# Kernel tuning notes

Hardware: AMD Instinct MI355X
Metric: run time of the kernel (lower is better)

Reference implementation:

```python
import jax, jax.numpy as jnp
import numpy as np

N = 50000      # nodes
E = 800000     # edges
F_IN = 128     # input_channels
H = 128        # hidden_channels
OUT = 10       # output_channels
G = 64         # graphs in batch


def setup_inputs() -> dict:
    key = jax.random.key(0)
    ks = jax.random.split(key, 16)
    s = 0.05
    inp = {
        "x": jax.random.normal(ks[0], (N, F_IN), jnp.float32),
        "edge_index": jax.random.randint(ks[1], (2, E), 0, N, jnp.int64 if jax.config.jax_enable_x64 else jnp.int32),
        "batch": jnp.sort(jax.random.randint(ks[2], (N,), 0, G, jnp.int32)),
        "conv1_w": jax.random.normal(ks[3], (F_IN, H), jnp.float32) * s,
        "conv1_b": jnp.zeros((H,), jnp.float32),
        "conv2_w": jax.random.normal(ks[4], (H, H), jnp.float32) * s,
        "conv2_b": jnp.zeros((H,), jnp.float32),
        "conv3_w": jax.random.normal(ks[5], (H, H), jnp.float32) * s,
        "conv3_b": jnp.zeros((H,), jnp.float32),
        "fc1_w": jax.random.normal(ks[6], (H, 8 * H), jnp.float32) * s,
        "fc1_b": jnp.zeros((8 * H,), jnp.float32),
        "fc2_w": jax.random.normal(ks[7], (8 * H, 4 * H), jnp.float32) * s,
        "fc2_b": jnp.zeros((4 * H,), jnp.float32),
        "fc3_w": jax.random.normal(ks[8], (4 * H, 2 * H), jnp.float32) * s,
        "fc3_b": jnp.zeros((2 * H,), jnp.float32),
        "fc4_w": jax.random.normal(ks[9], (2 * H, H), jnp.float32) * s,
        "fc4_b": jnp.zeros((H,), jnp.float32),
        "fc5_w": jax.random.normal(ks[10], (H, OUT), jnp.float32) * s,
        "fc5_b": jnp.zeros((OUT,), jnp.float32),
    }
    return inp


def _gcn_conv(x, w, b, src, dst, norm, n_nodes):
    # GCNConv: out = D^{-1/2} (A + I) D^{-1/2} X W + b   (self-loops already in src/dst)
    xw = x @ w                                        # [N, H]
    msg = xw[src] * norm[:, None]                     # gather + scale, [E+N, H]
    return jax.ops.segment_sum(msg, dst, num_segments=n_nodes) + b


def reference(x, edge_index, batch,
              conv1_w, conv1_b, conv2_w, conv2_b, conv3_w, conv3_b,
              fc1_w, fc1_b, fc2_w, fc2_b, fc3_w, fc3_b,
              fc4_w, fc4_b, fc5_w, fc5_b):
    n = x.shape[0]
    loop = jnp.arange(n, dtype=edge_index.dtype)
    src = jnp.concatenate([edge_index[0], loop])      # add self-loops
    dst = jnp.concatenate([edge_index[1], loop])
    deg = jax.ops.segment_sum(jnp.ones_like(dst, dtype=x.dtype), dst, num_segments=n)
    dinv = jnp.where(deg > 0, jax.lax.rsqrt(deg), 0.0)
    norm = dinv[src] * dinv[dst]                      # symmetric normalization per edge

    h = jax.nn.relu(_gcn_conv(x, conv1_w, conv1_b, src, dst, norm, n))
    h = jax.nn.relu(_gcn_conv(h, conv2_w, conv2_b, src, dst, norm, n))
    h = _gcn_conv(h, conv3_w, conv3_b, src, dst, norm, n)

    # global mean pool over graphs
    sums = jax.ops.segment_sum(h, batch, num_segments=G)
    cnt = jax.ops.segment_sum(jnp.ones((n,), x.dtype), batch, num_segments=G)
    f = sums / jnp.maximum(cnt, 1.0)[:, None]         # [G, H]

    y = jax.nn.relu(f @ fc1_w + fc1_b)
    y = jax.nn.relu(y @ fc2_w + fc2_b)
    y = jax.nn.relu(y @ fc3_w + fc3_b)
    y = jax.nn.relu(y @ fc4_w + fc4_b)
    # dropout p=0.5 is identity in eval mode
    y = y @ fc5_w + fc5_b                             # [G, OUT]
    return (f, y)
```

## Files before the change

### kernel.cpp

```cpp
#include <hip/hip_runtime.h>
#include <stdint.h>

#define N_NODES 50000
#define N_EDGES 800000
#define FEAT    128
#define NGRAPH  64

#define E_BLKS      3125
#define GSTRIP_BLKS 782
#define GR_BLKS     (GSTRIP_BLKS + E_BLKS)

typedef __attribute__((ext_vector_type(8))) short short8;
typedef __attribute__((ext_vector_type(4))) float floatx4;

static __device__ __forceinline__ ushort f2bf(float f) {
  uint32_t x = __float_as_uint(f);
  x += 0x7FFF + ((x >> 16) & 1);
  return (ushort)(x >> 16);
}
static __device__ __forceinline__ float bfLo(uint32_t u) {
  return __uint_as_float(u << 16);
}
static __device__ __forceinline__ float bfHi(uint32_t u) {
  return __uint_as_float(u & 0xFFFF0000u);
}

static __device__ __forceinline__ void cvt4T(const float* __restrict__ in,
                                             ushort* __restrict__ outT, int i) {
  float4 v = ((const float4*)in)[i];
  int k = (4 * i) >> 7;
  int n = (4 * i) & 127;
  outT[(size_t)(n + 0) * FEAT + k] = f2bf(v.x);
  outT[(size_t)(n + 1) * FEAT + k] = f2bf(v.y);
  outT[(size_t)(n + 2) * FEAT + k] = f2bf(v.z);
  outT[(size_t)(n + 3) * FEAT + k] = f2bf(v.w);
}

__global__ __launch_bounds__(256) void wcvt(const float* __restrict__ w0,
                                            const float* __restrict__ w1,
                                            ushort* __restrict__ wbT) {
  int i = blockIdx.x * 256 + threadIdx.x;
  if (i < 4096) cvt4T(w0, wbT, i);
  else cvt4T(w1, wbT + FEAT * FEAT, i - 4096);
}

static __device__ __forceinline__ void gemm_strip_f32a(int strip, int lane,
                                                       const float* __restrict__ X,
                                                       const ushort* __restrict__ WT,
                                                       ushort* __restrict__ XW) {
  if (strip >= N_NODES / 16) return;
  int m0 = strip * 16;
  int r = lane & 15, quad = lane >> 4;
  const float* xrow = X + (size_t)(m0 + r) * FEAT;
  short8 afr[4];
#pragma unroll
  for (int kb = 0; kb < 4; ++kb) {
    int k0 = kb * 32 + quad * 8;
    float4 f0 = *(const float4*)(xrow + k0);
    float4 f1 = *(const float4*)(xrow + k0 + 4);
    short8 a;
    a[0] = (short)f2bf(f0.x); a[1] = (short)f2bf(f0.y);
    a[2] = (short)f2bf(f0.z); a[3] = (short)f2bf(f0.w);
    a[4] = (short)f2bf(f1.x); a[5] = (short)f2bf(f1.y);
    a[6] = (short)f2bf(f1.z); a[7] = (short)f2bf(f1.w);
    afr[kb] = a;
  }
#pragma unroll
  for (int nt = 0; nt < 8; ++nt) {
    int n0 = nt * 16;
    floatx4 acc = {0.f, 0.f, 0.f, 0.f};
    const ushort* wrow = WT + (size_t)(n0 + r) * FEAT;
#pragma unroll
    for (int kb = 0; kb < 4; ++kb) {
      short8 b = *(const short8*)(wrow + kb * 32 + quad * 8);
      acc = __builtin_amdgcn_mfma_f32_16x16x32_bf16(afr[kb], b, acc, 0, 0, 0);
    }
#pragma unroll
    for (int reg = 0; reg < 4; ++reg)
      XW[(size_t)(m0 + quad * 4 + reg) * FEAT + n0 + r] = f2bf(acc[reg]);
  }
}

__global__ __launch_bounds__(256) void gemm_rank(const float* __restrict__ x,
                                                 const ushort* __restrict__ wbT,
                                                 ushort* __restrict__ msl,
                                                 const int* __restrict__ dst,
                                                 int* __restrict__ cnt,
                                                 int* __restrict__ rank) {
  int b = blockIdx.x, t = threadIdx.x;
  int fifth = b / 5;
  if (b - fifth * 5 == 0) {
    gemm_strip_f32a(fifth * 4 + (t >> 6), t & 63, x, wbT, msl);
  } else {
    int e = (b - fifth - 1) * 256 + t;
    rank[e] = atomicAdd(&cnt[dst[e]], 1);
  }
}

__global__ __launch_bounds__(256) void gemm2_strip(const ushort* __restrict__ X,
                                                   const ushort* __restrict__ WT,
                                                   ushort* __restrict__ XW) {
  int strip = (blockIdx.x * 256 + threadIdx.x) >> 6;
  int lane = threadIdx.x & 63;
  if (strip >= N_NODES / 16) return;
  int m0 = strip * 16;
  int r = lane & 15, quad = lane >> 4;
  const ushort* xrow = X + (size_t)(m0 + r) * FEAT;
  short8 afr[4];
#pragma unroll
  for (int kb = 0; kb < 4; ++kb)
    afr[kb] = *(const short8*)(xrow + kb * 32 + quad * 8);
#pragma unroll
  for (int nt = 0; nt < 8; ++nt) {
    int n0 = nt * 16;
    floatx4 acc = {0.f, 0.f, 0.f, 0.f};
    const ushort* wrow = WT + (size_t)(n0 + r) * FEAT;
#pragma unroll
    for (int kb = 0; kb < 4; ++kb) {
      short8 b = *(const short8*)(wrow + kb * 32 + quad * 8);
      acc = __builtin_amdgcn_mfma_f32_16x16x32_bf16(afr[kb], b, acc, 0, 0, 0);
    }
#pragma unroll
    for (int reg = 0; reg < 4; ++reg)
      XW[(size_t)(m0 + quad * 4 + reg) * FEAT + n0 + r] = f2bf(acc[reg]);
  }
}

__global__ __launch_bounds__(256) void dinv_scan1(const int* __restrict__ cnt,
                                                  const int* __restrict__ batch,
                                                  float* __restrict__ dinv,
                                                  float* __restrict__ cnt_g,
                                                  int* __restrict__ ptr,
                                                  int* __restrict__ bsums) {
  __shared__ int tmp[256];
  __shared__ int bins[NGRAPH];
  if (threadIdx.x < NGRAPH) bins[threadIdx.x] = 0;
  int i = blockIdx.x * 256 + threadIdx.x;
  int v = (i < N_NODES) ? cnt[i] : 0;
  tmp[threadIdx.x] = v;
  __syncthreads();
  for (int off = 1; off < 256; off <<= 1) {
    int t = (threadIdx.x >= off) ? tmp[threadIdx.x - off] : 0;
    __syncthreads();
    tmp[threadIdx.x] += t;
    __syncthreads();
  }
  if (i < N_NODES) ptr[i] = tmp[threadIdx.x] - v;
  if (threadIdx.x == 255) bsums[blockIdx.x] = tmp[255];
  if (i < N_NODES) {
    dinv[i] = rsqrtf((float)v + 1.0f);
    atomicAdd(&bins[batch[i]], 1);
  }
  __syncthreads();
  if (threadIdx.x < NGRAPH && bins[threadIdx.x] > 0)
    atomicAdd(&cnt_g[threadIdx.x], (float)bins[threadIdx.x]);
}

__global__ __launch_bounds__(256) void scan2(int* __restrict__ bsums, int nb) {
  __shared__ int tmp[256];
  int v = (threadIdx.x < nb) ? bsums[threadIdx.x] : 0;
  tmp[threadIdx.x] = v;
  __syncthreads();
  for (int off = 1; off < 256; off <<= 1) {
    int t = (threadIdx.x >= off) ? tmp[threadIdx.x - off] : 0;
    __syncthreads();
    tmp[threadIdx.x] += t;
    __syncthreads();
  }
  if (threadIdx.x < nb) bsums[threadIdx.x] = tmp[threadIdx.x] - v;
}

__global__ __launch_bounds__(256) void scan3(int* __restrict__ ptr,
                                             const int* __restrict__ bsums) {
  int i = blockIdx.x * 256 + threadIdx.x;
  if (i < N_NODES) ptr[i] += bsums[blockIdx.x];
}

__global__ __launch_bounds__(256) void fill_csr(const int* __restrict__ src,
                                                const int* __restrict__ dst,
                                                const int* __restrict__ rank,
                                                const int* __restrict__ ptr,
                                                const float* __restrict__ dinv,
                                                int2* __restrict__ edges) {
  int e = blockIdx.x * 256 + threadIdx.x;
  if (e >= N_EDGES) return;
  int s = src[e];
  edges[ptr[dst[e]] + rank[e]] = make_int2(s, __float_as_int(dinv[s]));
}

static __device__ __forceinline__ float2 agg_node(const uint32_t* __restrict__ m32,
                                                  const int2* __restrict__ edges,
                                                  int start, int n, int lane) {
  float ax0 = 0.f, ay0 = 0.f, ax1 = 0.f, ay1 = 0.f;
  float ax2 = 0.f, ay2 = 0.f, ax3 = 0.f, ay3 = 0.f;
  int i = 0;
  if ((start & 1) && n > 0) {
    int2 e = edges[start];
    uint32_t u = m32[(size_t)e.x * 64 + lane];
    float nrm = __int_as_float(e.y);
    ax0 = fmaf(nrm, bfLo(u), ax0);
    ay0 = fmaf(nrm, bfHi(u), ay0);
    i = 1;
  }
  for (; i + 8 <= n; i += 8) {
    const int4* ep = (const int4*)(edges + start + i);
    int4 q0 = ep[0], q1 = ep[1], q2 = ep[2], q3 = ep[3];
    uint32_t u0 = m32[(size_t)q0.x * 64 + lane];
    uint32_t u1 = m32[(size_t)q0.z * 64 + lane];
    uint32_t u2 = m32[(size_t)q1.x * 64 + lane];
    uint32_t u3 = m32[(size_t)q1.z * 64 + lane];
    uint32_t u4 = m32[(size_t)q2.x * 64 + lane];
    uint32_t u5 = m32[(size_t)q2.z * 64 + lane];
    uint32_t u6 = m32[(size_t)q3.x * 64 + lane];
    uint32_t u7 = m32[(size_t)q3.z * 64 + lane];
    float n0 = __int_as_float(q0.y), n1 = __int_as_float(q0.w);
    float n2 = __int_as_float(q1.y), n3 = __int_as_float(q1.w);
    float n4 = __int_as_float(q2.y), n5 = __int_as_float(q2.w);
    float n6 = __int_as_float(q3.y), n7 = __int_as_float(q3.w);
    ax0 = fmaf(n0, bfLo(u0), ax0); ay0 = fmaf(n0, bfHi(u0), ay0);
    ax1 = fmaf(n1, bfLo(u1), ax1); ay1 = fmaf(n1, bfHi(u1), ay1);
    ax2 = fmaf(n2, bfLo(u2), ax2); ay2 = fmaf(n2, bfHi(u2), ay2);
    ax3 = fmaf(n3, bfLo(u3), ax3); ay3 = fmaf(n3, bfHi(u3), ay3);
    ax0 = fmaf(n4, bfLo(u4), ax0); ay0 = fmaf(n4, bfHi(u4), ay0);
    ax1 = fmaf(n5, bfLo(u5), ax1); ay1 = fmaf(n5, bfHi(u5), ay1);
    ax2 = fmaf(n6, bfLo(u6), ax2); ay2 = fmaf(n6, bfHi(u6), ay2);
    ax3 = fmaf(n7, bfLo(u7), ax3); ay3 = fmaf(n7, bfHi(u7), ay3);
  }
  for (; i < n; ++i) {
    int2 e = edges[start + i];
    float nrm = __int_as_float(e.y);
    uint32_t u = m32[(size_t)e.x * 64 + lane];
    ax0 = fmaf(nrm, bfLo(u), ax0);
    ay0 = fmaf(nrm, bfHi(u), ay0);
  }
  return make_float2((ax0 + ax1) + (ax2 + ax3), (ay0 + ay1) + (ay2 + ay3));
}

template <int MODE>
__global__ __launch_bounds__(256) void agg_kernel(const ushort* __restrict__ msg,
                                                  const float* __restrict__ dinv,
                                                  const int* __restrict__ ptr,
                                                  const int* __restrict__ cnt,
                                                  const int2* __restrict__ edges,
                                                  const float* __restrict__ bias,
                                                  void* __restrict__ outp) {
  int wave = (blockIdx.x * 256 + threadIdx.x) >> 6;
  int lane = threadIdx.x & 63;
  if (wave >= N_NODES) return;
  int v = wave;
  float di = dinv[v];
  const uint32_t* m32 = (const uint32_t*)msg;
  uint32_t su = m32[(size_t)v * 64 + lane];
  float2 s = agg_node(m32, edges, ptr[v], cnt[v], lane);
  float ax = fmaf(di, bfLo(su), s.x);
  float ay = fmaf(di, bfHi(su), s.y);
  if (MODE == 2) {
    ((float2*)outp)[(size_t)v * 64 + lane] = make_float2(ax * di, ay * di);
  } else {
    ax = fmaf(ax, di, bias[2 * lane]);
    ay = fmaf(ay, di, bias[2 * lane + 1]);
    ushort2 h2;
    h2.x = f2bf(fmaxf(ax, 0.f));
    h2.y = f2bf(fmaxf(ay, 0.f));
    ((ushort2*)outp)[(size_t)v * 64 + lane] = h2;
  }
}

__global__ __launch_bounds__(256) void pool_sum(const float* __restrict__ a3,
                                                const int* __restrict__ batch,
                                                float* __restrict__ P) {
  int wave = blockIdx.x * 4 + (threadIdx.x >> 6);
  int lane = threadIdx.x & 63;
  int v0 = wave * 16;
  if (v0 >= N_NODES) return;
  int vend = v0 + 16;
  if (vend > N_NODES) vend = N_NODES;
  const float2* a2 = (const float2*)a3;
  float ax = 0.f, ay = 0.f;
  int g = batch[v0];
  for (int v = v0; v < vend; ++v) {
    int gv = batch[v];
    if (gv != g) {
      atomicAdd(&P[(size_t)g * FEAT + 2 * lane], ax);
      atomicAdd(&P[(size_t)g * FEAT + 2 * lane + 1], ay);
      ax = 0.f; ay = 0.f; g = gv;
    }
    float2 t = a2[(size_t)v * 64 + lane];
    ax += t.x;
    ay += t.y;
  }
  atomicAdd(&P[(size_t)g * FEAT + 2 * lane], ax);
  atomicAdd(&P[(size_t)g * FEAT + 2 * lane + 1], ay);
}

template <int K, int C, int KSLICE, int RELU_IN, int DIVC, int NSPLIT>
__global__ __launch_bounds__(256) void fc_layer(const float* __restrict__ IN,
                                                const float* __restrict__ W,
                                                const float* __restrict__ Bs,
                                                const float* __restrict__ cntg,
                                                float* __restrict__ OUT) {
  constexpr int CB = (C + 63) / 64;
  int lane = threadIdx.x & 63;
  int gq = threadIdx.x >> 6;
  int bid = blockIdx.x;
  int kp = bid % NSPLIT;
  int rest = bid / NSPLIT;
  int cg = rest % CB;
  int g = (rest / CB) * 4 + gq;
  int c = cg * 64 + lane;
  if (c >= C) return;
  int k0 = kp * KSLICE;
  const float* wp = W + (size_t)k0 * C + c;
  const float* in = IN + (size_t)g * K + k0;
  float cf = 1.f;
  if (DIVC) cf = fmaxf(cntg[g], 1.f);
  float a0 = 0.f, a1 = 0.f, a2 = 0.f, a3 = 0.f;
  float a4 = 0.f, a5 = 0.f, a6 = 0.f, a7 = 0.f;
#pragma unroll 2
  for (int k = 0; k < KSLICE; k += 8) {
    float i0 = in[k + 0], i1 = in[k + 1], i2 = in[k + 2], i3 = in[k + 3];
    float i4 = in[k + 4], i5 = in[k + 5], i6 = in[k + 6], i7 = in[k + 7];
    if (RELU_IN) {
      i0 = fmaxf(i0, 0.f); i1 = fmaxf(i1, 0.f);
      i2 = fmaxf(i2, 0.f); i3 = fmaxf(i3, 0.f);
      i4 = fmaxf(i4, 0.f); i5 = fmaxf(i5, 0.f);
      i6 = fmaxf(i6, 0.f); i7 = fmaxf(i7, 0.f);
    }
    if (DIVC) {
      i0 /= cf; i1 /= cf; i2 /= cf; i3 /= cf;
      i4 /= cf; i5 /= cf; i6 /= cf; i7 /= cf;
    }
    a0 = fmaf(i0, wp[(size_t)(k + 0) * C], a0);
    a1 = fmaf(i1, wp[(size_t)(k + 1) * C], a1);
    a2 = fmaf(i2, wp[(size_t)(k + 2) * C], a2);
    a3 = fmaf(i3, wp[(size_t)(k + 3) * C], a3);
    a4 = fmaf(i4, wp[(size_t)(k + 4) * C], a4);
    a5 = fmaf(i5, wp[(size_t)(k + 5) * C], a5);
    a6 = fmaf(i6, wp[(size_t)(k + 6) * C], a6);
    a7 = fmaf(i7, wp[(size_t)(k + 7) * C], a7);
  }
  float s = ((a0 + a1) + (a2 + a3)) + ((a4 + a5) + (a6 + a7));
  if (NSPLIT == 1) {
    OUT[(size_t)g * C + c] = s + Bs[c];
  } else {
    atomicAdd(&OUT[(size_t)g * C + c], s + (kp == 0 ? Bs[c] : 0.f));
  }
}

extern "C" void kernel_launch(void* const* d_in, const int* in_sizes, int n_in,
                              void* d_out, int out_size, void* d_ws, size_t ws_size,
                              hipStream_t stream) {
  const float* x         = (const float*)d_in[0];
  const int*   ei        = (const int*)d_in[1];
  const int*   batch     = (const int*)d_in[2];
  const float* conv_w[3] = {(const float*)d_in[3], (const float*)d_in[5], (const float*)d_in[7]};
  const float* conv_b[3] = {(const float*)d_in[4], (const float*)d_in[6], (const float*)d_in[8]};
  const float* fc_w[5]   = {(const float*)d_in[9],  (const float*)d_in[11],
                            (const float*)d_in[13], (const float*)d_in[15],
                            (const float*)d_in[17]};
  const float* fc_b[5]   = {(const float*)d_in[10], (const float*)d_in[12],
                            (const float*)d_in[14], (const float*)d_in[16],
                            (const float*)d_in[18]};
  const int* e_src = ei;
  const int* e_dst = ei + N_EDGES;
  float* out_f = (float*)d_out;
  float* out_y = (float*)d_out + NGRAPH * FEAT;

  char* p = (char*)d_ws;
  auto carve = [&](size_t bytes) {
    char* r = p;
    p += (bytes + 255) & ~(size_t)255;
    return r;
  };
  int*    cnt_i   = (int*)carve(N_NODES * 4);
  float*  dinv    = (float*)carve(N_NODES * 4);
  int*    csr_ptr = (int*)carve(N_NODES * 4);
  int*    bsums   = (int*)carve(256 * 4);
  int2*   edges   = (int2*)carve((size_t)N_EDGES * 8);
  ushort* wbT     = (ushort*)carve((size_t)2 * FEAT * FEAT * 2);
  ushort* hbuf    = (ushort*)carve((size_t)N_NODES * FEAT * 2);
  float*  f_sum   = (float*)carve(NGRAPH * FEAT * 4);
  float*  cnt_g   = (float*)carve(NGRAPH * 4);
  float*  Y1      = (float*)carve(NGRAPH * 1024 * 4);
  float*  Y2      = (float*)carve(NGRAPH * 512 * 4);
  float*  Y3      = (float*)carve(NGRAPH * 256 * 4);
  float*  Y4      = (float*)carve(NGRAPH * 128 * 4);
  char*   region  = carve((size_t)N_EDGES * 4 + 2 * (size_t)N_NODES * FEAT * 2);
  int*    rank    = (int*)region;
  ushort* msl1    = (ushort*)(region + (size_t)N_EDGES * 4);
  ushort* msl2    = (ushort*)(region + (size_t)N_EDGES * 4 + (size_t)N_NODES * FEAT * 2);
  float*  a3      = (float*)region;

  const int BLK_N = (N_NODES + 255) / 256;

  hipMemsetAsync(cnt_i, 0, N_NODES * 4, stream);
  hipMemsetAsync(f_sum, 0, NGRAPH * FEAT * 4 + 256, stream);
  hipMemsetAsync(Y2, 0, NGRAPH * (512 + 256 + 128) * 4, stream);

  wcvt<<<32, 256, 0, stream>>>(conv_w[0], conv_w[1], wbT);

  gemm_rank<<<GR_BLKS, 256, 0, stream>>>(x, wbT, msl1, e_dst, cnt_i, rank);

  dinv_scan1<<<BLK_N, 256, 0, stream>>>(cnt_i, batch, dinv, cnt_g, csr_ptr, bsums);
  scan2<<<1, 256, 0, stream>>>(bsums, BLK_N);
  scan3<<<BLK_N, 256, 0, stream>>>(csr_ptr, bsums);

  fill_csr<<<E_BLKS, 256, 0, stream>>>(e_src, e_dst, rank, csr_ptr, dinv, edges);

  const int AGG_BLKS  = (N_NODES + 3) / 4;
  const int POOL_BLKS = (N_NODES / 16 + 3) / 4 + 1;

  agg_kernel<0><<<AGG_BLKS, 256, 0, stream>>>(msl1, dinv, csr_ptr, cnt_i, edges,
                                              conv_b[0], hbuf);
  gemm2_strip<<<GSTRIP_BLKS, 256, 0, stream>>>(hbuf, wbT + FEAT * FEAT, msl2);
  agg_kernel<0><<<AGG_BLKS, 256, 0, stream>>>(msl2, dinv, csr_ptr, cnt_i, edges,
                                              conv_b[1], hbuf);
  agg_kernel<2><<<AGG_BLKS, 256, 0, stream>>>(hbuf, dinv, csr_ptr, cnt_i, edges,
                                              nullptr, a3);
  pool_sum<<<POOL_BLKS, 256, 0, stream>>>(a3, batch, f_sum);

  fc_layer< 128, 128, 128, 0, 1, 1><<< 32, 256, 0, stream>>>(f_sum, conv_w[2], conv_b[2], cnt_g, out_f);
  fc_layer< 128,1024, 128, 0, 0, 1><<<256, 256, 0, stream>>>(out_f, fc_w[0], fc_b[0], nullptr, Y1);
  fc_layer<1024, 512, 256, 1, 0, 4><<<512, 256, 0, stream>>>(Y1, fc_w[1], fc_b[1], nullptr, Y2);
  fc_layer< 512, 256, 128, 1, 0, 4><<<256, 256, 0, stream>>>(Y2, fc_w[2], fc_b[2], nullptr, Y3);
  fc_layer< 256, 128,  32, 1, 0, 8><<<256, 256, 0, stream>>>(Y3, fc_w[3], fc_b[3], nullptr, Y4);
  fc_layer< 128,  10, 128, 1, 0, 1><<< 16, 256, 0, stream>>>(Y4, fc_w[4], fc_b[4], nullptr, out_y);
}
```

Before: 369.5 us.

## Split GCN aggregation into two feature-plane passes with half-wave edge parallelism

Each aggregation layer now launches twice, each pass handling 64 of the 128 features. Within a wave the two 32-lane halves process alternating edges and combine results with a cross-half shuffle. The aim is to shrink the gathered feature working set per pass for better cache hit rates. In exchange, edge-list reads and launch count double, and half the lanes are idle at the store.

```diff
diff --git a/kernel.cpp b/kernel.cpp
--- a/kernel.cpp
+++ b/kernel.cpp
@@ -188,81 +188,82 @@
   edges[ptr[dst[e]] + rank[e]] = make_int2(s, __float_as_int(dinv[s]));
 }
 
-static __device__ __forceinline__ float2 agg_node(const uint32_t* __restrict__ m32,
-                                                  const int2* __restrict__ edges,
-                                                  int start, int n, int lane) {
-  float ax0 = 0.f, ay0 = 0.f, ax1 = 0.f, ay1 = 0.f;
-  float ax2 = 0.f, ay2 = 0.f, ax3 = 0.f, ay3 = 0.f;
-  int i = 0;
-  if ((start & 1) && n > 0) {
-    int2 e = edges[start];
-    uint32_t u = m32[(size_t)e.x * 64 + lane];
-    float nrm = __int_as_float(e.y);
-    ax0 = fmaf(nrm, bfLo(u), ax0);
-    ay0 = fmaf(nrm, bfHi(u), ay0);
-    i = 1;
-  }
-  for (; i + 8 <= n; i += 8) {
-    const int4* ep = (const int4*)(edges + start + i);
-    int4 q0 = ep[0], q1 = ep[1], q2 = ep[2], q3 = ep[3];
-    uint32_t u0 = m32[(size_t)q0.x * 64 + lane];
-    uint32_t u1 = m32[(size_t)q0.z * 64 + lane];
-    uint32_t u2 = m32[(size_t)q1.x * 64 + lane];
-    uint32_t u3 = m32[(size_t)q1.z * 64 + lane];
-    uint32_t u4 = m32[(size_t)q2.x * 64 + lane];
-    uint32_t u5 = m32[(size_t)q2.z * 64 + lane];
-    uint32_t u6 = m32[(size_t)q3.x * 64 + lane];
-    uint32_t u7 = m32[(size_t)q3.z * 64 + lane];
-    float n0 = __int_as_float(q0.y), n1 = __int_as_float(q0.w);
-    float n2 = __int_as_float(q1.y), n3 = __int_as_float(q1.w);
-    float n4 = __int_as_float(q2.y), n5 = __int_as_float(q2.w);
-    float n6 = __int_as_float(q3.y), n7 = __int_as_float(q3.w);
-    ax0 = fmaf(n0, bfLo(u0), ax0); ay0 = fmaf(n0, bfHi(u0), ay0);
-    ax1 = fmaf(n1, bfLo(u1), ax1); ay1 = fmaf(n1, bfHi(u1), ay1);
-    ax2 = fmaf(n2, bfLo(u2), ax2); ay2 = fmaf(n2, bfHi(u2), ay2);
-    ax3 = fmaf(n3, bfLo(u3), ax3); ay3 = fmaf(n3, bfHi(u3), ay3);
-    ax0 = fmaf(n4, bfLo(u4), ax0); ay0 = fmaf(n4, bfHi(u4), ay0);
-    ax1 = fmaf(n5, bfLo(u5), ax1); ay1 = fmaf(n5, bfHi(u5), ay1);
-    ax2 = fmaf(n6, bfLo(u6), ax2); ay2 = fmaf(n6, bfHi(u6), ay2);
-    ax3 = fmaf(n7, bfLo(u7), ax3); ay3 = fmaf(n7, bfHi(u7), ay3);
-  }
-  for (; i < n; ++i) {
-    int2 e = edges[start + i];
-    float nrm = __int_as_float(e.y);
-    uint32_t u = m32[(size_t)e.x * 64 + lane];
-    ax0 = fmaf(nrm, bfLo(u), ax0);
-    ay0 = fmaf(nrm, bfHi(u), ay0);
-  }
-  return make_float2((ax0 + ax1) + (ax2 + ax3), (ay0 + ay1) + (ay2 + ay3));
-}
-
-template <int MODE>
-__global__ __launch_bounds__(256) void agg_kernel(const ushort* __restrict__ msg,
-                                                  const float* __restrict__ dinv,
-                                                  const int* __restrict__ ptr,
-                                                  const int* __restrict__ cnt,
-                                                  const int2* __restrict__ edges,
-                                                  const float* __restrict__ bias,
-                                                  void* __restrict__ outp) {
+template <int MODE, int PLANE>
+__global__ __launch_bounds__(256) void agg_split(const ushort* __restrict__ msg,
+                                                 const float* __restrict__ dinv,
+                                                 const int* __restrict__ ptr,
+                                                 const int* __restrict__ cnt,
+                                                 const int2* __restrict__ edges,
+                                                 const float* __restrict__ bias,
+                                                 void* __restrict__ outp) {
   int wave = (blockIdx.x * 256 + threadIdx.x) >> 6;
   int lane = threadIdx.x & 63;
   if (wave >= N_NODES) return;
   int v = wave;
+  int half = lane >> 5, l5 = lane & 31;
   float di = dinv[v];
   const uint32_t* m32 = (const uint32_t*)msg;
-  uint32_t su = m32[(size_t)v * 64 + lane];
-  float2 s = agg_node(m32, edges, ptr[v], cnt[v], lane);
-  float ax = fmaf(di, bfLo(su), s.x);
-  float ay = fmaf(di, bfHi(su), s.y);
-  if (MODE == 2) {
-    ((float2*)outp)[(size_t)v * 64 + lane] = make_float2(ax * di, ay * di);
-  } else {
-    ax = fmaf(ax, di, bias[2 * lane]);
-    ay = fmaf(ay, di, bias[2 * lane + 1]);
-    ushort2 h2;
-    h2.x = f2bf(fmaxf(ax, 0.f));
-    h2.y = f2bf(fmaxf(ay, 0.f));
-    ((ushort2*)outp)[(size_t)v * 64 + lane] = h2;
+  uint32_t su = m32[(size_t)v * 64 + PLANE * 32 + l5];
+  int start = ptr[v];
+  int n = cnt[v];
+  float a0l = 0.f, a0h = 0.f, a1l = 0.f, a1h = 0.f;
+  float a2l = 0.f, a2h = 0.f, a3l = 0.f, a3h = 0.f;
+  int i = 0;
+  if ((start & 1) && n > 0) {
+    int2 e = edges[start];
+    float nrm = half ? 0.f : __int_as_float(e.y);
+    uint32_t u = m32[(size_t)e.x * 64 + PLANE * 32 + l5];
+    a0l = fmaf(nrm, bfLo(u), a0l);
+    a0h = fmaf(nrm, bfHi(u), a0h);
+    i = 1;
+  }
+  for (; i + 8 <= n; i += 8) {
+    const int4* ep = (const int4*)(edges + start + i);
+    int4 q0 = ep[0], q1 = ep[1], q2 = ep[2], q3 = ep[3];
+    int s0 = half ? q0.z : q0.x;
+    int s1 = half ? q1.z : q1.x;
+    int s2 = half ? q2.z : q2.x;
+    int s3 = half ? q3.z : q3.x;
+    float n0 = __int_as_float(half ? q0.w : q0.y);
+    float n1 = __int_as_float(half ? q1.w : q1.y);
+    float n2 = __int_as_float(half ? q2.w : q2.y);
+    float n3 = __int_as_float(half ? q3.w : q3.y);
+    uint32_t u0 = m32[(size_t)s0 * 64 + PLANE * 32 + l5];
+    uint32_t u1 = m32[(size_t)s1 * 64 + PLANE * 32 + l5];
+    uint32_t u2 = m32[(size_t)s2 * 64 + PLANE * 32 + l5];
+    uint32_t u3 = m32[(size_t)s3 * 64 + PLANE * 32 + l5];
+    a0l = fmaf(n0, bfLo(u0), a0l); a0h = fmaf(n0, bfHi(u0), a0h);
+    a1l = fmaf(n1, bfLo(u1), a1l); a1h = fmaf(n1, bfHi(u1), a1h);
+    a2l = fmaf(n2, bfLo(u2), a2l); a2h = fmaf(n2, bfHi(u2), a2h);
+    a3l = fmaf(n3, bfLo(u3), a3l); a3h = fmaf(n3, bfHi(u3), a3h);
+  }
+  for (; i < n; i += 2) {
+    int j = i + half;
+    int2 e = edges[start + (j < n ? j : i)];
+    float nrm = (j < n) ? __int_as_float(e.y) : 0.f;
+    uint32_t u = m32[(size_t)e.x * 64 + PLANE * 32 + l5];
+    a0l = fmaf(nrm, bfLo(u), a0l);
+    a0h = fmaf(nrm, bfHi(u), a0h);
+  }
+  float sl = (a0l + a1l) + (a2l + a3l);
+  float sh = (a0h + a1h) + (a2h + a3h);
+  sl += __shfl_xor(sl, 32);
+  sh += __shfl_xor(sh, 32);
+  float ax = fmaf(di, bfLo(su), sl);
+  float ay = fmaf(di, bfHi(su), sh);
+  if (lane < 32) {
+    int idx = v * 64 + PLANE * 32 + l5;
+    if (MODE == 2) {
+      ((float2*)outp)[idx] = make_float2(ax * di, ay * di);
+    } else {
+      int f = PLANE * 32 + l5;
+      ax = fmaf(ax, di, bias[2 * f]);
+      ay = fmaf(ay, di, bias[2 * f + 1]);
+      ushort2 h2;
+      h2.x = f2bf(fmaxf(ax, 0.f));
+      h2.y = f2bf(fmaxf(ay, 0.f));
+      ((ushort2*)outp)[idx] = h2;
+    }
   }
 }
 
@@ -410,13 +411,19 @@
   const int AGG_BLKS  = (N_NODES + 3) / 4;
   const int POOL_BLKS = (N_NODES / 16 + 3) / 4 + 1;
 
-  agg_kernel<0><<<AGG_BLKS, 256, 0, stream>>>(msl1, dinv, csr_ptr, cnt_i, edges,
-                                              conv_b[0], hbuf);
+  agg_split<0, 0><<<AGG_BLKS, 256, 0, stream>>>(msl1, dinv, csr_ptr, cnt_i, edges,
+                                                conv_b[0], hbuf);
+  agg_split<0, 1><<<AGG_BLKS, 256, 0, stream>>>(msl1, dinv, csr_ptr, cnt_i, edges,
+                                                conv_b[0], hbuf);
   gemm2_strip<<<GSTRIP_BLKS, 256, 0, stream>>>(hbuf, wbT + FEAT * FEAT, msl2);
-  agg_kernel<0><<<AGG_BLKS, 256, 0, stream>>>(msl2, dinv, csr_ptr, cnt_i, edges,
-                                              conv_b[1], hbuf);
-  agg_kernel<2><<<AGG_BLKS, 256, 0, stream>>>(hbuf, dinv, csr_ptr, cnt_i, edges,
-                                              nullptr, a3);
+  agg_split<0, 0><<<AGG_BLKS, 256, 0, stream>>>(msl2, dinv, csr_ptr, cnt_i, edges,
+                                                conv_b[1], hbuf);
+  agg_split<0, 1><<<AGG_BLKS, 256, 0, stream>>>(msl2, dinv, csr_ptr, cnt_i, edges,
+                                                conv_b[1], hbuf);
+  agg_split<2, 0><<<AGG_BLKS, 256, 0, stream>>>(hbuf, dinv, csr_ptr, cnt_i, edges,
+                                                nullptr, a3);
+  agg_split<2, 1><<<AGG_BLKS, 256, 0, stream>>>(hbuf, dinv, csr_ptr, cnt_i, edges,
+                                                nullptr, a3);
   pool_sum<<<POOL_BLKS, 256, 0, stream>>>(a3, batch, f_sum);
 
   fc_layer< 128, 128, 128, 0, 1, 1><<< 32, 256, 0, stream>>>(f_sum, conv_w[2], conv_b[2], cnt_g, out_f);
```

New measurement: 427.8 us. +15.8%, slower.
